# Performance work log

Hardware: AMD Instinct MI355X
Metric: run time of the kernel (lower is better)

## Reference

```python
import jax, jax.numpy as jnp
import numpy as np

N, D, H, O, E = 50000, 512, 512, 256, 150000
NEG_SLOPE = 0.2
EPS = 1e-16


def gat_conv(x, edge_index, W_src, W_dst, a_src, a_dst, bias):
    """Single-head PyG GATConv, add_self_loops=False.
    x: [N, Din]; edge_index: [2, E] (row 0 = src, row 1 = dst).
    W_src/W_dst: [Din, C]; a_src/a_dst: [C]; bias: [C].
    """
    src, dst = edge_index[0], edge_index[1]
    h_src = x @ W_src                      # [N, C]
    h_dst = x @ W_dst                      # [N, C]
    alpha_src = h_src @ a_src              # [N]
    alpha_dst = h_dst @ a_dst              # [N]
    e = jax.nn.leaky_relu(alpha_src[src] + alpha_dst[dst], NEG_SLOPE)  # [E]
    # per-destination segment softmax (numerically stable)
    m = jax.ops.segment_max(e, dst, num_segments=N)       # [N]
    ex = jnp.exp(e - m[dst])                               # [E]
    s = jax.ops.segment_sum(ex, dst, num_segments=N)       # [N]
    alpha = ex / (s[dst] + EPS)                            # [E]
    # scatter-add weighted source messages to destinations
    out = jax.ops.segment_sum(alpha[:, None] * h_src[src], dst, num_segments=N)  # [N, C]
    return out + bias


def setup_inputs() -> dict:
    key = jax.random.key(0)
    ks = jax.random.split(key, 20)
    g = lambda i, shape, sc: (jax.random.normal(ks[i], shape, dtype=jnp.float32) * sc)
    inp = {
        "x": jax.random.normal(ks[0], (N, D), dtype=jnp.float32),
        "edge_index": jax.random.randint(ks[1], (2, E), 0, N, dtype=jnp.int32),
        "edge_index_2_hop": jax.random.randint(ks[2], (2, E), 0, N, dtype=jnp.int32),
        # conv1 (D -> H)
        "W1_src": g(3, (D, H), 0.05), "W1_dst": g(4, (D, H), 0.05),
        "a1_src": g(5, (H,), 0.05), "a1_dst": g(6, (H,), 0.05),
        "b1": jnp.zeros((H,), jnp.float32),
        # lin1 (H -> H)
        "Wl1": g(7, (H, H), 0.05), "bl1": jnp.zeros((H,), jnp.float32),
        # conv2 (H -> O)
        "W2_src": g(8, (H, O), 0.05), "W2_dst": g(9, (H, O), 0.05),
        "a2_src": g(10, (O,), 0.05), "a2_dst": g(11, (O,), 0.05),
        "b2": jnp.zeros((O,), jnp.float32),
        # lin2 (O -> O)
        "Wl2": g(12, (O, O), 0.05), "bl2": jnp.zeros((O,), jnp.float32),
    }
    return inp


def reference(x, edge_index, edge_index_2_hop,
              W1_src, W1_dst, a1_src, a1_dst, b1, Wl1, bl1,
              W2_src, W2_dst, a2_src, a2_dst, b2, Wl2, bl2):
    h = (gat_conv(x, edge_index, W1_src, W1_dst, a1_src, a1_dst, b1)
         + gat_conv(x, edge_index_2_hop, W1_src, W1_dst, a1_src, a1_dst, b1))
    h = jax.nn.relu(h @ Wl1 + bl1)
    h = (gat_conv(h, edge_index, W2_src, W2_dst, a2_src, a2_dst, b2)
         + gat_conv(h, edge_index_2_hop, W2_src, W2_dst, a2_src, a2_dst, b2))
    return h @ Wl2 + bl2
```

## Files before the change

kernel.cpp:

```cpp
#include <hip/hip_runtime.h>

typedef unsigned short u16;
typedef __attribute__((ext_vector_type(8))) unsigned short v8u16;
typedef __attribute__((ext_vector_type(4))) unsigned short v4u16;
typedef __attribute__((ext_vector_type(8))) __bf16 v8bf;
typedef __attribute__((ext_vector_type(4))) float v4f;

#define NN 50000
#define EE 150000
#define SCAN_CHUNK 512
#define NB_PER_SET 98

__device__ inline float b2f(u16 u) {
    union { unsigned int i; float f; } x; x.i = ((unsigned int)u) << 16; return x.f;
}
__device__ inline u16 f2b(float f) {
    union { float f; unsigned int i; } x; x.f = f;
    unsigned int r = x.i + 0x7FFFu + ((x.i >> 16) & 1u);
    return (u16)(r >> 16);
}
__device__ inline float wred(float v) {
    v += __shfl_down(v, 32, 64);
    v += __shfl_down(v, 16, 64);
    v += __shfl_down(v, 8, 64);
    v += __shfl_down(v, 4, 64);
    v += __shfl_down(v, 2, 64);
    v += __shfl_down(v, 1, 64);
    return v;
}
__device__ inline int wred_i(int v) {
    v += __shfl_down(v, 32, 64);
    v += __shfl_down(v, 16, 64);
    v += __shfl_down(v, 8, 64);
    v += __shfl_down(v, 4, 64);
    v += __shfl_down(v, 2, 64);
    v += __shfl_down(v, 1, 64);
    return v;
}

__device__ __forceinline__ void gll16(const u16* g, u16* l) {
    __builtin_amdgcn_global_load_lds(
        (const __attribute__((address_space(1))) void*)g,
        (__attribute__((address_space(3))) void*)l, 16, 0, 0);
}


__global__ void transpose4(const float* __restrict__ W0, u16* __restrict__ T0,
                           const float* __restrict__ W1, u16* __restrict__ T1,
                           const float* __restrict__ W2, u16* __restrict__ T2,
                           const float* __restrict__ W3, u16* __restrict__ T3) {
    int idx = blockIdx.x * blockDim.x + threadIdx.x;
    const float* W; u16* T; int N, K, base;
    if (idx < 262144)      { W = W0; T = T0; K = 512; N = 512; base = 0; }
    else if (idx < 524288) { W = W1; T = T1; K = 512; N = 512; base = 262144; }
    else if (idx < 655360) { W = W2; T = T2; K = 512; N = 256; base = 524288; }
    else if (idx < 720896) { W = W3; T = T3; K = 256; N = 256; base = 655360; }
    else return;
    int i = idx - base;
    int n = i % N, k = i / N;
    T[(size_t)n * K + k] = f2b(W[i]);
}

__global__ void wv4(const float* __restrict__ Wa, const float* __restrict__ Wb,
                    const float* __restrict__ Wc, const float* __restrict__ Wd,
                    const float* __restrict__ aa, const float* __restrict__ ab,
                    const float* __restrict__ ac, const float* __restrict__ ad,
                    float* __restrict__ vbuf) {
    int rw = (blockIdx.x * blockDim.x + threadIdx.x) >> 6;
    int lane = threadIdx.x & 63;
    if (rw >= 2048) return;
    int seg = rw >> 9, r = rw & 511;
    const float* W; const float* a; int C;
    if (seg == 0)      { W = Wa; a = aa; C = 512; }
    else if (seg == 1) { W = Wb; a = ab; C = 512; }
    else if (seg == 2) { W = Wc; a = ac; C = 256; }
    else               { W = Wd; a = ad; C = 256; }
    float s = 0.f;
    int c0 = lane * 8;
    if (c0 < C) {
        const float* wp = W + (size_t)r * C + c0;
        v4f w0 = *(const v4f*)wp;
        v4f w1 = *(const v4f*)(wp + 4);
        v4f a0 = *(const v4f*)(a + c0);
        v4f a1 = *(const v4f*)(a + c0 + 4);
#pragma unroll
        for (int j = 0; j < 4; ++j) s += w0[j] * a0[j] + w1[j] * a1[j];
    }
    s = wred(s);
    if (lane == 0) vbuf[rw] = s;
}

__global__ void alpha_pair_f32x(const float* __restrict__ X, const float* __restrict__ vs,
                                const float* __restrict__ vd, float* __restrict__ as_,
                                float* __restrict__ ad_, u16* __restrict__ Xb, int Nn) {
    int w = (blockIdx.x * blockDim.x + threadIdx.x) >> 6;
    int lane = threadIdx.x & 63;
    if (w >= Nn) return;
    const float* xp = X + (size_t)w * 512 + lane * 8;
    v4f x0 = *(const v4f*)xp;
    v4f x1 = *(const v4f*)(xp + 4);
    const float* vsp = vs + lane * 8;
    const float* vdp = vd + lane * 8;
    float s1 = 0.f, s2 = 0.f;
    v8u16 o;
#pragma unroll
    for (int j = 0; j < 4; ++j) {
        s1 += x0[j] * vsp[j] + x1[j] * vsp[j + 4];
        s2 += x0[j] * vdp[j] + x1[j] * vdp[j + 4];
        o[j] = f2b(x0[j]); o[j + 4] = f2b(x1[j]);
    }
    *(v8u16*)(Xb + (size_t)w * 512 + lane * 8) = o;
    s1 = wred(s1);
    s2 = wred(s2);
    if (lane == 0) { as_[w] = s1; ad_[w] = s2; }
}


__global__ void deg2_kernel(const int* __restrict__ ei1, const int* __restrict__ ei2,
                            int* __restrict__ deg) {
    int idx = blockIdx.x * blockDim.x + threadIdx.x;
    if (idx >= 2 * EE) return;
    int set = idx >= EE;
    int e = idx - set * EE;
    const int* ei = set ? ei2 : ei1;
    atomicAdd(&deg[set * NN + ei[EE + e]], 1);
}

__global__ void scan_partial(const int* __restrict__ deg, int* __restrict__ bsum) {
    int b = blockIdx.x;
    int set = b / NB_PER_SET, lb = b - set * NB_PER_SET;
    int tid = threadIdx.x;
    int i0 = lb * SCAN_CHUNK + tid * 2;
    int s = 0;
    if (i0 < NN)     s += deg[set * NN + i0];
    if (i0 + 1 < NN) s += deg[set * NN + i0 + 1];
    s = wred_i(s);
    __shared__ int lsum[4];
    if ((tid & 63) == 0) lsum[tid >> 6] = s;
    __syncthreads();
    if (tid == 0) bsum[b] = lsum[0] + lsum[1] + lsum[2] + lsum[3];
}

__global__ void scan_tops(int* __restrict__ bsum) {
    __shared__ int ls[256];
    int tid = threadIdx.x;
    int set = tid >> 7, lb = tid & 127;
    int v = (lb < NB_PER_SET) ? bsum[set * NB_PER_SET + lb] : 0;
    ls[tid] = v;
    __syncthreads();
    for (int off = 1; off < 128; off <<= 1) {
        int t = (lb >= off) ? ls[tid - off] : 0;
        __syncthreads();
        ls[tid] += t;
        __syncthreads();
    }
    if (lb < NB_PER_SET) bsum[set * NB_PER_SET + lb] = ls[tid] - v;
}

__global__ void scan_final(const int* __restrict__ deg, const int* __restrict__ bsum,
                           int* __restrict__ rp) {
    int b = blockIdx.x;
    int set = b / NB_PER_SET, lb = b - set * NB_PER_SET;
    int tid = threadIdx.x;
    int i0 = lb * SCAN_CHUNK + tid * 2;
    int d0 = (i0 < NN)     ? deg[set * NN + i0]     : 0;
    int d1 = (i0 + 1 < NN) ? deg[set * NN + i0 + 1] : 0;
    int pair = d0 + d1;
    __shared__ int ps[256];
    ps[tid] = pair;
    __syncthreads();
    for (int off = 1; off < 256; off <<= 1) {
        int t = (tid >= off) ? ps[tid - off] : 0;
        __syncthreads();
        ps[tid] += t;
        __syncthreads();
    }
    int base = bsum[b] + ps[tid] - pair;
    if (i0 < NN)     rp[set * (NN + 1) + i0] = base;
    if (i0 + 1 < NN) rp[set * (NN + 1) + i0 + 1] = base + d0;
    if (b == 0 && tid == 0) { rp[NN] = EE; rp[(NN + 1) + NN] = EE; }
}

__global__ void fill2_kernel(const int* __restrict__ ei1, const int* __restrict__ ei2,
                             const int* __restrict__ rp, int* __restrict__ deg,
                             int* __restrict__ srcp, int* __restrict__ dstp) {
    int idx = blockIdx.x * blockDim.x + threadIdx.x;
    if (idx >= 2 * EE) return;
    int set = idx >= EE;
    int e = idx - set * EE;
    const int* ei = set ? ei2 : ei1;
    int d = ei[EE + e];
    int old = atomicSub(&deg[set * NN + d], 1);
    int pos = rp[set * (NN + 1) + d] + old - 1;
    srcp[set * EE + pos] = ei[e];
    dstp[set * EE + pos] = d;
}

__global__ void edge_ex(const int* __restrict__ srcp, const int* __restrict__ dstp,
                        const float* __restrict__ asrc, const float* __restrict__ adst,
                        float* __restrict__ ex) {
    int i = blockIdx.x * blockDim.x + threadIdx.x;
    if (i >= 2 * EE) return;
    float t = asrc[srcp[i]] + adst[dstp[i]];
    t = t > 0.f ? t : 0.2f * t;
    ex[i] = __expf(fminf(t, 60.f));
}

template <int CV>
__global__ void gat_pull(const int* __restrict__ rp, const int* __restrict__ srcp,
                         const float* __restrict__ ex, const u16* __restrict__ H,
                         const float* __restrict__ bias, u16* __restrict__ G, int Nn) {
    const int C = CV * 64;
    int d = (blockIdx.x * blockDim.x + threadIdx.x) >> 6;
    int lane = threadIdx.x & 63;
    if (d >= Nn) return;
    float out[CV];
#pragma unroll
    for (int j = 0; j < CV; ++j) out[j] = 0.f;
#pragma unroll
    for (int set = 0; set < 2; ++set) {
        const int* rpS = rp + set * (NN + 1);
        int base = set * EE;
        int beg = rpS[d], end = rpS[d + 1];
        float acc[CV];
#pragma unroll
        for (int j = 0; j < CV; ++j) acc[j] = 0.f;
        float ssum = 0.f;
        for (int i = beg; i < end; ++i) {
            float w = ex[base + i];
            int s = srcp[base + i];
            ssum += w;
            const u16* hp = H + (size_t)s * C + lane * CV;
            if constexpr (CV == 8) {
                v8u16 hv = *(const v8u16*)hp;
#pragma unroll
                for (int j = 0; j < 8; ++j) acc[j] += w * b2f(hv[j]);
            } else {
                v4u16 hv = *(const v4u16*)hp;
#pragma unroll
                for (int j = 0; j < 4; ++j) acc[j] += w * b2f(hv[j]);
            }
        }
        float inv = 1.f / (ssum + 1e-16f);
#pragma unroll
        for (int j = 0; j < CV; ++j) out[j] += acc[j] * inv;
    }
    const float* bp = bias + lane * CV;
    u16* gp = G + (size_t)d * C + lane * CV;
    if constexpr (CV == 8) {
        v8u16 o;
#pragma unroll
        for (int j = 0; j < 8; ++j) o[j] = f2b(out[j] + 2.f * bp[j]);
        *(v8u16*)gp = o;
    } else {
        v4u16 o;
#pragma unroll
        for (int j = 0; j < 4; ++j) o[j] = f2b(out[j] + 2.f * bp[j]);
        *(v4u16*)gp = o;
    }
}

__global__ __launch_bounds__(256, 2) void gemm_bf16(
    const u16* __restrict__ A, const u16* __restrict__ Bt, void* __restrict__ Cv,
    int M, int N, int K, const float* __restrict__ bias, int relu, int outf32,
    const float* __restrict__ avs, const float* __restrict__ avd,
    float* __restrict__ aout_s, float* __restrict__ aout_d) {
    __shared__ u16 As[2][128 * 32];
    __shared__ u16 Bs[2][128 * 32];
    const int tid = threadIdx.x;
    const int lane = tid & 63;
    const int wid = tid >> 6;
    const int wm = wid >> 1;
    const int wn = wid & 1;
    const int quad = lane >> 4;
    const int l16 = lane & 15;

    const int nwg = gridDim.x * gridDim.y;
    const int orig = blockIdx.y * gridDim.x + blockIdx.x;
    const int q = nwg >> 3, r = nwg & 7;
    const int xcd = orig & 7, loc = orig >> 3;
    const int wg = (xcd < r ? xcd * (q + 1) : r * (q + 1) + (xcd - r) * q) + loc;
    const int tileM = (wg / gridDim.x) * 128;
    const int tileN = (wg % gridDim.x) * 128;

    const int srow = tid >> 2;
    const int scol = (tid & 3) * 8;
    int ra0 = tileM + srow;       if (ra0 >= M) ra0 = M - 1;
    int ra1 = tileM + 64 + srow;  if (ra1 >= M) ra1 = M - 1;
    const u16* gA0 = A + (size_t)ra0 * K + scol;
    const u16* gA1 = A + (size_t)ra1 * K + scol;
    const u16* gB0 = Bt + (size_t)(tileN + srow) * K + scol;
    const u16* gB1 = Bt + (size_t)(tileN + 64 + srow) * K + scol;

    v4f acc[4][4];
#pragma unroll
    for (int i = 0; i < 4; ++i)
#pragma unroll
        for (int j = 0; j < 4; ++j) acc[i][j] = v4f{0.f, 0.f, 0.f, 0.f};

    const int nt = K >> 5;
    gll16(gA0, &As[0][wid * 512]);
    gll16(gA1, &As[0][2048 + wid * 512]);
    gll16(gB0, &Bs[0][wid * 512]);
    gll16(gB1, &Bs[0][2048 + wid * 512]);
    __syncthreads();

    int cur = 0;
    for (int t = 0; t < nt; ++t) {
        if (t + 1 < nt) {
            int kk = (t + 1) << 5;
            gll16(gA0 + kk, &As[cur ^ 1][wid * 512]);
            gll16(gA1 + kk, &As[cur ^ 1][2048 + wid * 512]);
            gll16(gB0 + kk, &Bs[cur ^ 1][wid * 512]);
            gll16(gB1 + kk, &Bs[cur ^ 1][2048 + wid * 512]);
        }
        v8bf af[4], bfr[4];
#pragma unroll
        for (int i = 0; i < 4; ++i)
            af[i] = __builtin_bit_cast(v8bf, *(const v8u16*)&As[cur][(wm * 64 + i * 16 + l16) * 32 + quad * 8]);
#pragma unroll
        for (int i = 0; i < 4; ++i)
            bfr[i] = __builtin_bit_cast(v8bf, *(const v8u16*)&Bs[cur][(wn * 64 + i * 16 + l16) * 32 + quad * 8]);
#pragma unroll
        for (int mi = 0; mi < 4; ++mi)
#pragma unroll
            for (int ni = 0; ni < 4; ++ni)
                acc[mi][ni] = __builtin_amdgcn_mfma_f32_16x16x32_bf16(af[mi], bfr[ni], acc[mi][ni], 0, 0, 0);
        __syncthreads();
        cur ^= 1;
    }

    float rs[4][4], rd[4][4];
#pragma unroll
    for (int mi = 0; mi < 4; ++mi)
#pragma unroll
        for (int rr = 0; rr < 4; ++rr) { rs[mi][rr] = 0.f; rd[mi][rr] = 0.f; }

#pragma unroll
    for (int mi = 0; mi < 4; ++mi)
#pragma unroll
        for (int ni = 0; ni < 4; ++ni) {
            int col = tileN + wn * 64 + ni * 16 + l16;
            float bb = bias ? bias[col] : 0.f;
            float ws_ = avs ? avs[col] : 0.f;
            float wd_ = avd ? avd[col] : 0.f;
            int row0 = tileM + wm * 64 + mi * 16 + quad * 4;
#pragma unroll
            for (int rr = 0; rr < 4; ++rr) {
                int row = row0 + rr;
                if (row < M) {
                    float v = acc[mi][ni][rr] + bb;
                    if (relu) v = fmaxf(v, 0.f);
                    if (outf32) ((float*)Cv)[(size_t)row * N + col] = v;
                    else        ((u16*)Cv)[(size_t)row * N + col] = f2b(v);
                    rs[mi][rr] += v * ws_;
                    rd[mi][rr] += v * wd_;
                }
            }
        }

    if (avs) {
#pragma unroll
        for (int mi = 0; mi < 4; ++mi)
#pragma unroll
            for (int rr = 0; rr < 4; ++rr) {
                int row = tileM + wm * 64 + mi * 16 + quad * 4 + rr;
                float a = rs[mi][rr], b = rd[mi][rr];
                a += __shfl_down(a, 8, 64); a += __shfl_down(a, 4, 64);
                a += __shfl_down(a, 2, 64); a += __shfl_down(a, 1, 64);
                b += __shfl_down(b, 8, 64); b += __shfl_down(b, 4, 64);
                b += __shfl_down(b, 2, 64); b += __shfl_down(b, 1, 64);
                if (l16 == 0 && row < M) {
                    atomicAdd(&aout_s[row], a);
                    atomicAdd(&aout_d[row], b);
                }
            }
    }
}


extern "C" void kernel_launch(void* const* d_in, const int* in_sizes, int n_in,
                              void* d_out, int out_size, void* d_ws, size_t ws_size,
                              hipStream_t stream) {
    const float* x  = (const float*)d_in[0];
    const int* ei1  = (const int*)d_in[1];
    const int* ei2  = (const int*)d_in[2];
    const float* W1s = (const float*)d_in[3];
    const float* W1d = (const float*)d_in[4];
    const float* a1s = (const float*)d_in[5];
    const float* a1d = (const float*)d_in[6];
    const float* b1  = (const float*)d_in[7];
    const float* Wl1 = (const float*)d_in[8];
    const float* bl1 = (const float*)d_in[9];
    const float* W2s = (const float*)d_in[10];
    const float* W2d = (const float*)d_in[11];
    const float* a2s = (const float*)d_in[12];
    const float* a2d = (const float*)d_in[13];
    const float* b2  = (const float*)d_in[14];
    const float* Wl2 = (const float*)d_in[15];
    const float* bl2 = (const float*)d_in[16];
    float* out = (float*)d_out;

    char* ws = (char*)d_ws;
    size_t off = 0;
    auto alloc = [&](size_t b) { void* p = ws + off; off = (off + b + 255) & ~(size_t)255; return p; };
    u16* bufA   = (u16*)alloc((size_t)NN * 512 * 2);
    u16* bufB   = (u16*)alloc((size_t)NN * 512 * 2);
    int* rp     = (int*)alloc((size_t)2 * (NN + 1) * 4);
    int* srcp   = (int*)alloc((size_t)2 * EE * 4);
    int* dstp   = (int*)alloc((size_t)2 * EE * 4);
    int* deg    = (int*)alloc((size_t)2 * NN * 4);
    int* bsum   = (int*)alloc((size_t)2 * NB_PER_SET * 4);
    float* ex   = (float*)alloc((size_t)2 * EE * 4);
    float* asrc = (float*)alloc((size_t)NN * 4);
    float* adst = (float*)alloc((size_t)NN * 4);
    float* vbuf = (float*)alloc(2048 * 4);
    u16* Wt1s   = (u16*)alloc((size_t)512 * 512 * 2);
    u16* Wtl1   = (u16*)alloc((size_t)512 * 512 * 2);
    u16* Wt2s   = (u16*)alloc((size_t)512 * 256 * 2);
    u16* Wtl2   = (u16*)alloc((size_t)256 * 256 * 2);
    u16* g2buf  = bufB + (size_t)NN * 256;

    hipMemsetAsync(deg, 0, (size_t)2 * NN * 4, stream);
    deg2_kernel<<<(2 * EE + 255) / 256, 256, 0, stream>>>(ei1, ei2, deg);
    scan_partial<<<2 * NB_PER_SET, 256, 0, stream>>>(deg, bsum);
    scan_tops<<<1, 256, 0, stream>>>(bsum);
    scan_final<<<2 * NB_PER_SET, 256, 0, stream>>>(deg, bsum, rp);
    fill2_kernel<<<(2 * EE + 255) / 256, 256, 0, stream>>>(ei1, ei2, rp, deg, srcp, dstp);

    transpose4<<<(720896 + 255) / 256, 256, 0, stream>>>(W1s, Wt1s, Wl1, Wtl1, W2s, Wt2s, Wl2, Wtl2);
    wv4<<<512, 256, 0, stream>>>(W1s, W1d, W2s, W2d, a1s, a1d, a2s, a2d, vbuf);

    alpha_pair_f32x<<<(NN + 3) / 4, 256, 0, stream>>>(x, vbuf, vbuf + 512, asrc, adst, bufB, NN);
    edge_ex<<<(2 * EE + 255) / 256, 256, 0, stream>>>(srcp, dstp, asrc, adst, ex);
    gemm_bf16<<<dim3(4, 391), 256, 0, stream>>>(bufB, Wt1s, bufA, NN, 512, 512, nullptr, 0, 0,
                                                nullptr, nullptr, nullptr, nullptr);
    gat_pull<8><<<(NN + 3) / 4, 256, 0, stream>>>(rp, srcp, ex, bufA, b1, bufB, NN);
    hipMemsetAsync(asrc, 0, (size_t)NN * 4, stream);
    hipMemsetAsync(adst, 0, (size_t)NN * 4, stream);
    gemm_bf16<<<dim3(4, 391), 256, 0, stream>>>(bufB, Wtl1, bufA, NN, 512, 512, bl1, 1, 0,
                                                vbuf + 1024, vbuf + 1536, asrc, adst);

    edge_ex<<<(2 * EE + 255) / 256, 256, 0, stream>>>(srcp, dstp, asrc, adst, ex);
    gemm_bf16<<<dim3(2, 391), 256, 0, stream>>>(bufA, Wt2s, bufB, NN, 256, 512, nullptr, 0, 0,
                                                nullptr, nullptr, nullptr, nullptr);
    gat_pull<4><<<(NN + 3) / 4, 256, 0, stream>>>(rp, srcp, ex, bufB, b2, g2buf, NN);
    gemm_bf16<<<dim3(2, 391), 256, 0, stream>>>(g2buf, Wtl2, out, NN, 256, 256, bl2, 0, 1,
                                                nullptr, nullptr, nullptr, nullptr);

    (void)in_sizes; (void)n_in; (void)out_size; (void)ws_size;
}
```

Baseline: 524.6 us.

## Use XOR-swizzled 64-wide K tiles in GEMM, dropping double buffering

The bf16 GEMM now stages a 128x64 K-slab per iteration instead of double-buffered 128x32 slabs. An XOR swizzle on the LDS column blocks is meant to avoid bank conflicts on the fragment reads. Each slab feeds two MFMA k-steps, halving the number of barrier-separated iterations. In exchange, the next tile is no longer prefetched while computing, so global load latency is exposed at every iteration. The swizzle also changes which global column each thread loads, so correctness depends on the LDS layout matching the read pattern.

```diff
diff --git a/kernel.cpp b/kernel.cpp
--- a/kernel.cpp
+++ b/kernel.cpp
@@ -265,8 +265,8 @@
     int M, int N, int K, const float* __restrict__ bias, int relu, int outf32,
     const float* __restrict__ avs, const float* __restrict__ avd,
     float* __restrict__ aout_s, float* __restrict__ aout_d) {
-    __shared__ u16 As[2][128 * 32];
-    __shared__ u16 Bs[2][128 * 32];
+    __shared__ u16 As[128 * 64];
+    __shared__ u16 Bs[128 * 64];
     const int tid = threadIdx.x;
     const int lane = tid & 63;
     const int wid = tid >> 6;
@@ -283,14 +283,28 @@
     const int tileM = (wg / gridDim.x) * 128;
     const int tileN = (wg % gridDim.x) * 128;
 
-    const int srow = tid >> 2;
-    const int scol = (tid & 3) * 8;
+    const int srow = tid >> 3;
+    const int scol = 8 * ((tid & 7) ^ ((tid >> 3) & 7));
     int ra0 = tileM + srow;       if (ra0 >= M) ra0 = M - 1;
-    int ra1 = tileM + 64 + srow;  if (ra1 >= M) ra1 = M - 1;
+    int ra1 = tileM + 32 + srow;  if (ra1 >= M) ra1 = M - 1;
+    int ra2 = tileM + 64 + srow;  if (ra2 >= M) ra2 = M - 1;
+    int ra3 = tileM + 96 + srow;  if (ra3 >= M) ra3 = M - 1;
     const u16* gA0 = A + (size_t)ra0 * K + scol;
     const u16* gA1 = A + (size_t)ra1 * K + scol;
+    const u16* gA2 = A + (size_t)ra2 * K + scol;
+    const u16* gA3 = A + (size_t)ra3 * K + scol;
     const u16* gB0 = Bt + (size_t)(tileN + srow) * K + scol;
-    const u16* gB1 = Bt + (size_t)(tileN + 64 + srow) * K + scol;
+    const u16* gB1 = Bt + (size_t)(tileN + 32 + srow) * K + scol;
+    const u16* gB2 = Bt + (size_t)(tileN + 64 + srow) * K + scol;
+    const u16* gB3 = Bt + (size_t)(tileN + 96 + srow) * K + scol;
+    u16* lA0 = As + 0 * 2048 + wid * 512;
+    u16* lA1 = As + 1 * 2048 + wid * 512;
+    u16* lA2 = As + 2 * 2048 + wid * 512;
+    u16* lA3 = As + 3 * 2048 + wid * 512;
+    u16* lB0 = Bs + 0 * 2048 + wid * 512;
+    u16* lB1 = Bs + 1 * 2048 + wid * 512;
+    u16* lB2 = Bs + 2 * 2048 + wid * 512;
+    u16* lB3 = Bs + 3 * 2048 + wid * 512;
 
     v4f acc[4][4];
 #pragma unroll
@@ -298,36 +312,35 @@
 #pragma unroll
         for (int j = 0; j < 4; ++j) acc[i][j] = v4f{0.f, 0.f, 0.f, 0.f};
 
-    const int nt = K >> 5;
-    gll16(gA0, &As[0][wid * 512]);
-    gll16(gA1, &As[0][2048 + wid * 512]);
-    gll16(gB0, &Bs[0][wid * 512]);
-    gll16(gB1, &Bs[0][2048 + wid * 512]);
-    __syncthreads();
-
-    int cur = 0;
-    for (int t = 0; t < nt; ++t) {
-        if (t + 1 < nt) {
-            int kk = (t + 1) << 5;
-            gll16(gA0 + kk, &As[cur ^ 1][wid * 512]);
-            gll16(gA1 + kk, &As[cur ^ 1][2048 + wid * 512]);
-            gll16(gB0 + kk, &Bs[cur ^ 1][wid * 512]);
-            gll16(gB1 + kk, &Bs[cur ^ 1][2048 + wid * 512]);
+    for (int k0 = 0; k0 < K; k0 += 64) {
+        gll16(gA0 + k0, lA0);
+        gll16(gA1 + k0, lA1);
+        gll16(gA2 + k0, lA2);
+        gll16(gA3 + k0, lA3);
+        gll16(gB0 + k0, lB0);
+        gll16(gB1 + k0, lB1);
+        gll16(gB2 + k0, lB2);
+        gll16(gB3 + k0, lB3);
+        __syncthreads();
+#pragma unroll
+        for (int ks = 0; ks < 2; ++ks) {
+            const int cblk = ((((ks << 2) | quad) ^ (l16 & 7)) << 3);
+            v8bf af[4], bfr[4];
+#pragma unroll
+            for (int i = 0; i < 4; ++i)
+                af[i] = __builtin_bit_cast(v8bf,
+                    *(const v8u16*)&As[(wm * 64 + i * 16 + l16) * 64 + cblk]);
+#pragma unroll
+            for (int i = 0; i < 4; ++i)
+                bfr[i] = __builtin_bit_cast(v8bf,
+                    *(const v8u16*)&Bs[(wn * 64 + i * 16 + l16) * 64 + cblk]);
+#pragma unroll
+            for (int mi = 0; mi < 4; ++mi)
+#pragma unroll
+                for (int ni = 0; ni < 4; ++ni)
+                    acc[mi][ni] = __builtin_amdgcn_mfma_f32_16x16x32_bf16(af[mi], bfr[ni], acc[mi][ni], 0, 0, 0);
         }
-        v8bf af[4], bfr[4];
-#pragma unroll
-        for (int i = 0; i < 4; ++i)
-            af[i] = __builtin_bit_cast(v8bf, *(const v8u16*)&As[cur][(wm * 64 + i * 16 + l16) * 32 + quad * 8]);
-#pragma unroll
-        for (int i = 0; i < 4; ++i)
-            bfr[i] = __builtin_bit_cast(v8bf, *(const v8u16*)&Bs[cur][(wn * 64 + i * 16 + l16) * 32 + quad * 8]);
-#pragma unroll
-        for (int mi = 0; mi < 4; ++mi)
-#pragma unroll
-            for (int ni = 0; ni < 4; ++ni)
-                acc[mi][ni] = __builtin_amdgcn_mfma_f32_16x16x32_bf16(af[mi], bfr[ni], acc[mi][ni], 0, 0, 0);
-        __syncthreads();
-        cur ^= 1;
+        __syncthreads();
     }
 
     float rs[4][4], rd[4][4];
```

After: 517.7 us. About the same (-1.3%).
